# Optimization experiments

Hardware: AMD Instinct MI355X
Metric: run time of the kernel (lower is better)

The kernel has to match this reference:

```python
import jax, jax.numpy as jnp
import numpy as np

FEAT_STRIDE = 16
A = 4  # num anchors (forced by scores.view(-1, K, 4))
FRAMES_PER_VIDEO = 300


def conv2d(x, w, b, pad):
    y = jax.lax.conv_general_dilated(
        x, w, window_strides=(1, 1), padding=[(pad, pad), (pad, pad)],
        dimension_numbers=("NCHW", "OIHW", "NCHW"))
    return y + b[None, :, None, None]


def setup_inputs() -> dict:
    key = jax.random.key(0)
    ks = jax.random.split(key, 8)
    B, C, H, W = 300, 256, 38, 38
    base_feat = jax.random.normal(ks[0], (B, C, H, W), dtype=jnp.float32)
    central_pos = jax.random.randint(ks[1], (1,), 0, FRAMES_PER_VIDEO)
    im_info = jnp.ones((1,), dtype=jnp.float32)
    gt_boxes = jax.random.uniform(ks[2], (1, 4), dtype=jnp.float32)
    # learned params
    W1 = jax.random.normal(ks[3], (128, C, 2, 2), dtype=jnp.float32) * 0.05
    b1 = jnp.zeros((128,), dtype=jnp.float32)
    Wc = jax.random.normal(ks[4], (2 * A, 128, 2, 2), dtype=jnp.float32) * 0.05
    bc = jnp.zeros((2 * A,), dtype=jnp.float32)
    Wb = jax.random.normal(ks[5], (4 * A, 128, 2, 2), dtype=jnp.float32) * 0.05
    bb = jnp.zeros((4 * A,), dtype=jnp.float32)
    anchors = jnp.array([[-8., -8., 8., 8.], [-16., -16., 16., 16.],
                         [-32., -32., 32., 32.], [-64., -64., 64., 64.]],
                        dtype=jnp.float32)
    return {"base_feat": base_feat, "central_pos": central_pos,
            "im_info": im_info, "gt_boxes": gt_boxes,
            "W1": W1, "b1": b1, "Wc": Wc, "bc": bc, "Wb": Wb, "bb": bb,
            "anchors": anchors}


def reference(base_feat, central_pos, im_info, gt_boxes, W1, b1, Wc, bc, Wb, bb, anchors):
    x = jax.nn.relu(conv2d(base_feat, W1, b1, pad=1))          # [B,128,H+1,W+1]
    cls = conv2d(x, Wc, bc, pad=0)                             # [B,2A,H,W]
    B, _, H, Wd = cls.shape
    # torch reshape(x, 2) -> softmax -> reshape back (raw row-major reshapes)
    prob = jax.nn.softmax(cls.reshape(B, 2, A * H, Wd), axis=1).reshape(B, 2 * A, H, Wd)
    scores = prob[:, A:]                                       # [B,A,H,W]
    deltas = conv2d(x, Wb, bb, pad=0)                          # [B,4A,H,W]
    K = H * Wd
    sx = jnp.arange(Wd, dtype=jnp.float32) * FEAT_STRIDE
    sy = jnp.arange(H, dtype=jnp.float32) * FEAT_STRIDE
    gx, gy = jnp.meshgrid(sx, sy)                              # [H,W] each ('xy')
    shifts = jnp.stack([gx.ravel(), gy.ravel(), gx.ravel(), gy.ravel()], axis=1)  # [K,4]
    props = (anchors[None, :, :] + shifts[:, None, :]).reshape(K * A, 4)[None]    # [1,K*A,4]
    d = deltas.transpose(0, 2, 3, 1).reshape(B, K * A, 4)
    proposals = (props + d) * im_info                          # [B,K*A,4]
    # raw reshape of [B,A,H,W] into [B,K,4] (matches .view semantics on a copy)
    sk = scores.reshape(B, K, 4)
    sf = sk.max(axis=2)
    of = sk.argmax(axis=2)                                     # [B,K]
    ss = sf.max(axis=1)
    os_ = sf.argmax(axis=1)                                    # [B]
    bi = jnp.arange(B)
    box_id = os_ * 4 + of[bi, os_]
    boxes = proposals[bi, box_id]                              # [B,4]
    anchor_out = jnp.trunc(boxes / im_info)                    # .int() cast (trunc)
    output = jnp.concatenate([anchor_out, boxes, ss[:, None]], axis=1)  # [B,9]
    # log loss at central frames (vectorized over videos)
    nv = gt_boxes.shape[0]
    idx = FRAMES_PER_VIDEO * jnp.arange(nv) + central_pos
    valid = idx < B
    idxc = jnp.clip(idx, 0, B - 1)
    vb = boxes[idxc]
    vs = ss[idxc]
    # faithful IoU (including the original's max-instead-of-min on xi2/yi2)
    xi1 = jnp.maximum(gt_boxes[:, 0], vb[:, 0])
    yi1 = jnp.maximum(gt_boxes[:, 1], vb[:, 1])
    xi2 = jnp.maximum(gt_boxes[:, 2], vb[:, 2])
    yi2 = jnp.maximum(gt_boxes[:, 3], vb[:, 3])
    inter = (xi2 - xi1) * (yi2 - yi1)
    a1 = (gt_boxes[:, 2] - gt_boxes[:, 0]) * (gt_boxes[:, 3] - gt_boxes[:, 1])
    a2 = (vb[:, 2] - vb[:, 0]) * (vb[:, 3] - vb[:, 1])
    iou = inter / (a1 + a2 - inter)
    lv = jnp.where(iou > 0.7, -jnp.log(vs + 1e-5), -jnp.log(1.0 - vs + 1e-5))
    proposal_loss = jnp.sum(jnp.where(valid, lv, 0.0))
    return output, proposal_loss
```

## Files before the change

kernel.cpp:

```cpp
#include <hip/hip_runtime.h>
#include <math.h>

#define CIN 256
#define HIN 38
#define WIN 38
#define NFRAMES 300
#define COUT1 128
#define P1 1521
#define PSTR 1524
#define HW2 1444
#define NSC 5776
#define CHUNK 75
#define NCHUNKS 4
#define W1F_LO 131072
#define W2F_LO 16384

typedef _Float16 half8 __attribute__((ext_vector_type(8)));
typedef _Float16 half2v __attribute__((ext_vector_type(2)));
typedef float    f32x4 __attribute__((ext_vector_type(4)));

union H2U { unsigned int u; half2v h; };

#define LDS_BAR() do { \
    asm volatile("s_waitcnt lgkmcnt(0)" ::: "memory"); \
    __builtin_amdgcn_s_barrier(); \
    asm volatile("" ::: "memory"); \
} while (0)

__global__ void repack_w1f(const float* __restrict__ W1, _Float16* __restrict__ W1f) {
    int e = blockIdx.x * 256 + threadIdx.x;
    int j  = e & 7;
    int ln = (e >> 3) & 63;
    int mt = (e >> 9) & 7;
    int s  = e >> 12;
    int k  = s * 32 + (ln >> 4) * 8 + j;
    int co = mt * 16 + (ln & 15);
    int kid = k & 3, ci = k >> 2;
    float v = W1[((co * 256) + ci) * 4 + kid] * 64.0f;
    _Float16 h = (_Float16)v;
    W1f[e]          = h;
    W1f[e + W1F_LO] = (_Float16)(v - (float)h);
}

__global__ void repack_w2f(const float* __restrict__ Wc, const float* __restrict__ Wb,
                           _Float16* __restrict__ W2f) {
    int e = blockIdx.x * 256 + threadIdx.x;
    int j  = e & 7;
    int ln = (e >> 3) & 63;
    int mt = (e >> 9) & 1;
    int s  = e >> 10;
    int k  = s * 32 + (ln >> 4) * 8 + j;
    int ch = mt * 16 + (ln & 15);
    int ci = k >> 2, kid = k & 3;
    float v = 0.0f;
    if (ch < 8)       v = Wc[(ch * 128 + ci) * 4 + kid];
    else if (ch < 24) v = Wb[((ch - 8) * 128 + ci) * 4 + kid];
    v *= 64.0f;
    _Float16 h = (_Float16)v;
    W2f[e]          = h;
    W2f[e + W2F_LO] = (_Float16)(v - (float)h);
}

__global__ __launch_bounds__(256, 2) void conv1_mfma(
    const float* __restrict__ bf, const _Float16* __restrict__ W1f,
    const float* __restrict__ b1, unsigned int* __restrict__ xout, int frame0)
{
    __shared__ __align__(16) _Float16 As[16384];
    __shared__ __align__(16) _Float16 Bs[16384];

    const int tid  = threadIdx.x;
    const int wave = tid >> 6, ln = tid & 63;
    const int wrow = wave >> 1, wcol = wave & 1;
    const int fz = blockIdx.y;
    const int b  = frame0 + fz;
    const int p0 = blockIdx.x * 128;
    const float* bfb = bf + (size_t)b * (CIN * HIN * WIN);

    int  addr1[2][8];
    bool kok[2][4];
    int  saddr[2];
#pragma unroll
    for (int r = 0; r < 2; ++r) {
        int slot = tid + r * 256;
        int ln_s = slot & 63, nt = slot >> 6;
        int p = p0 + nt * 16 + (ln_s & 15);
        int quad = ln_s >> 4;
        bool pok = p < P1;
        int pp = pok ? p : 0;
        int h = pp / 39, w = pp - h * 39;
#pragma unroll
        for (int kid = 0; kid < 4; ++kid) {
            int hh = h + (kid >> 1) - 1;
            int ww = w + (kid & 1) - 1;
            kok[r][kid] = pok && ((unsigned)hh < 38u) && ((unsigned)ww < 38u);
            int ko = hh * 38 + ww;
#pragma unroll
            for (int t = 0; t < 2; ++t)
                addr1[r][t * 4 + kid] = quad * 2 * 1444 + t * 1444 + ko;
        }
        saddr[r] = slot * 8;
    }

    f32x4 acc[4][4];
#pragma unroll
    for (int i = 0; i < 4; ++i)
#pragma unroll
        for (int j = 0; j < 4; ++j) acc[i][j] = (f32x4)0.0f;

    float bn0[2][8], bn1[2][8];
    half8 an0[4], an1[4];

#define C1_LOAD(SET, S) do { \
        const float* bsrc_ = bfb + (size_t)(S) * 8 * 1444; \
        _Pragma("unroll") \
        for (int r_ = 0; r_ < 2; ++r_) { \
            _Pragma("unroll") \
            for (int j_ = 0; j_ < 8; ++j_) \
                bn##SET[r_][j_] = kok[r_][j_ & 3] ? bsrc_[addr1[r_][j_]] : 0.0f; \
        } \
        const _Float16* wsl_ = W1f + (size_t)(S) * 4096; \
        _Pragma("unroll") \
        for (int f_ = 0; f_ < 4; ++f_) { \
            int o_ = (tid + f_ * 256) * 8; \
            const _Float16* g_ = (f_ < 2) ? (wsl_ + o_) : (wsl_ + W1F_LO + (o_ - 4096)); \
            an##SET[f_] = *(const half8*)g_; \
        } \
    } while (0)

#define C1_STORE(SET, BUF) do { \
        const int bo_ = (BUF) * 8192; \
        _Pragma("unroll") \
        for (int r_ = 0; r_ < 2; ++r_) { \
            half8 hv_, lv_; \
            _Pragma("unroll") \
            for (int j_ = 0; j_ < 8; ++j_) { \
                float v_ = bn##SET[r_][j_] * 32.0f; \
                _Float16 h_ = (_Float16)v_; \
                hv_[j_] = h_; lv_[j_] = (_Float16)(v_ - (float)h_); \
            } \
            *(half8*)&Bs[bo_ + saddr[r_]] = hv_; \
            *(half8*)&Bs[bo_ + 4096 + saddr[r_]] = lv_; \
        } \
        _Pragma("unroll") \
        for (int f_ = 0; f_ < 4; ++f_) \
            *(half8*)&As[bo_ + (tid + f_ * 256) * 8] = an##SET[f_]; \
    } while (0)

#define C1_COMPUTE(BUF) do { \
        const int bo_ = (BUF) * 8192; \
        half8 af_h[4], af_l[4], bf_h[4], bf_l[4]; \
        _Pragma("unroll") \
        for (int t_ = 0; t_ < 4; ++t_) { \
            int mtile_ = wrow * 4 + t_; \
            af_h[t_] = *(const half8*)&As[bo_ + mtile_ * 512 + ln * 8]; \
            af_l[t_] = *(const half8*)&As[bo_ + 4096 + mtile_ * 512 + ln * 8]; \
            int ntile_ = wcol * 4 + t_; \
            bf_h[t_] = *(const half8*)&Bs[bo_ + (ntile_ * 64 + ln) * 8]; \
            bf_l[t_] = *(const half8*)&Bs[bo_ + 4096 + (ntile_ * 64 + ln) * 8]; \
        } \
        __builtin_amdgcn_s_setprio(1); \
        _Pragma("unroll") \
        for (int i_ = 0; i_ < 4; ++i_) { \
            _Pragma("unroll") \
            for (int j_ = 0; j_ < 4; ++j_) \
                acc[i_][j_] = __builtin_amdgcn_mfma_f32_16x16x32_f16(af_h[i_], bf_h[j_], acc[i_][j_], 0, 0, 0); \
        } \
        _Pragma("unroll") \
        for (int i_ = 0; i_ < 4; ++i_) { \
            _Pragma("unroll") \
            for (int j_ = 0; j_ < 4; ++j_) \
                acc[i_][j_] = __builtin_amdgcn_mfma_f32_16x16x32_f16(af_l[i_], bf_h[j_], acc[i_][j_], 0, 0, 0); \
        } \
        _Pragma("unroll") \
        for (int i_ = 0; i_ < 4; ++i_) { \
            _Pragma("unroll") \
            for (int j_ = 0; j_ < 4; ++j_) \
                acc[i_][j_] = __builtin_amdgcn_mfma_f32_16x16x32_f16(af_h[i_], bf_l[j_], acc[i_][j_], 0, 0, 0); \
        } \
        __builtin_amdgcn_s_setprio(0); \
    } while (0)

    C1_LOAD(0, 0);
    C1_LOAD(1, 1);
    C1_STORE(0, 0);
    LDS_BAR();

    for (int s = 0; s < 32; s += 2) {
        if (s + 2 < 32) C1_LOAD(0, s + 2);
        C1_COMPUTE(0);
        C1_STORE(1, 1);
        LDS_BAR();
        if (s + 3 < 32) C1_LOAD(1, s + 3);
        C1_COMPUTE(1);
        if (s + 2 < 32) {
            C1_STORE(0, 0);
            LDS_BAR();
        }
    }
#undef C1_LOAD
#undef C1_STORE
#undef C1_COMPUTE

    const float sc = 1.0f / 2048.0f;
    const int rq = ln >> 4, cl = ln & 15;
#pragma unroll
    for (int i = 0; i < 4; ++i) {
#pragma unroll
        for (int j = 0; j < 4; ++j) {
            int p = p0 + (wcol * 4 + j) * 16 + cl;
            if (p < P1) {
#pragma unroll
                for (int rr = 0; rr < 4; ++rr) {
                    int co = (wrow * 4 + i) * 16 + rq * 4 + rr;
                    float t = fmaxf(fmaf(acc[i][j][rr], sc, b1[co]), 0.0f) * 32.0f;
                    H2U u;
                    u.h[0] = (_Float16)t;
                    u.h[1] = (_Float16)(t - (float)u.h[0]);
                    xout[((size_t)fz * COUT1 + co) * PSTR + p] = u.u;
                }
            }
        }
    }
}

__global__ __launch_bounds__(256, 2) void stage2_mfma(
    const unsigned int* __restrict__ xq, const _Float16* __restrict__ W2f,
    const float* __restrict__ bcv, const float* __restrict__ bbv,
    float* __restrict__ scores, float* __restrict__ deltas, int frame0)
{
    __shared__ __align__(16) _Float16 Bs[16384];
    __shared__ float clsb[8][128];

    const int tid  = threadIdx.x;
    const int wave = tid >> 6, ln = tid & 63;
    const int fz = blockIdx.y;
    const int b  = frame0 + fz;
    const int p0 = blockIdx.x * 128;
    const unsigned int* xb = xq + (size_t)fz * COUT1 * PSTR;

    int  addr2[2][8];
    bool sok[2];
    int  saddr[2];
#pragma unroll
    for (int r = 0; r < 2; ++r) {
        int slot = tid + r * 256;
        int ln_s = slot & 63, nt = slot >> 6;
        int p = p0 + nt * 16 + (ln_s & 15);
        int quad = ln_s >> 4;
        sok[r] = p < HW2;
        int pp = sok[r] ? p : 0;
        int h = pp / 38, w = pp - h * 38;
#pragma unroll
        for (int kid = 0; kid < 4; ++kid) {
            int ko = (h + (kid >> 1)) * 39 + (w + (kid & 1));
#pragma unroll
            for (int t = 0; t < 2; ++t)
                addr2[r][t * 4 + kid] = (quad * 2 + t) * PSTR + ko;
        }
        saddr[r] = slot * 8;
    }

    f32x4 acc[2][2];
    acc[0][0] = (f32x4)0.0f; acc[0][1] = (f32x4)0.0f;
    acc[1][0] = (f32x4)0.0f; acc[1][1] = (f32x4)0.0f;

    unsigned int bu0[2][8], bu1[2][8];
    half8 a0_h[2], a0_l[2], a1_h[2], a1_l[2];

#define S2_LOADB(SET, S) do { \
        const unsigned int* row_ = xb + (size_t)(S) * 8 * PSTR; \
        _Pragma("unroll") \
        for (int r_ = 0; r_ < 2; ++r_) { \
            _Pragma("unroll") \
            for (int j_ = 0; j_ < 8; ++j_) \
                bu##SET[r_][j_] = sok[r_] ? row_[addr2[r_][j_]] : 0u; \
        } \
    } while (0)

#define S2_LOADA(SET, S) do { \
        _Pragma("unroll") \
        for (int mt_ = 0; mt_ < 2; ++mt_) { \
            const _Float16* wp_ = W2f + ((size_t)((S) * 2 + mt_) * 64 + ln) * 8; \
            a##SET##_h[mt_] = *(const half8*)wp_; \
            a##SET##_l[mt_] = *(const half8*)(wp_ + W2F_LO); \
        } \
    } while (0)

#define S2_STORE(SET, BUF) do { \
        const int bo_ = (BUF) * 8192; \
        _Pragma("unroll") \
        for (int r_ = 0; r_ < 2; ++r_) { \
            half8 hv_, lv_; \
            _Pragma("unroll") \
            for (int j_ = 0; j_ < 8; ++j_) { \
                H2U t_; t_.u = bu##SET[r_][j_]; \
                hv_[j_] = t_.h[0]; lv_[j_] = t_.h[1]; \
            } \
            *(half8*)&Bs[bo_ + saddr[r_]] = hv_; \
            *(half8*)&Bs[bo_ + 4096 + saddr[r_]] = lv_; \
        } \
    } while (0)

#define S2_COMPUTE(SET, BUF) do { \
        const int bo_ = (BUF) * 8192; \
        half8 b_h[2], b_l[2]; \
        _Pragma("unroll") \
        for (int t_ = 0; t_ < 2; ++t_) { \
            int ntile_ = wave * 2 + t_; \
            b_h[t_] = *(const half8*)&Bs[bo_ + (ntile_ * 64 + ln) * 8]; \
            b_l[t_] = *(const half8*)&Bs[bo_ + 4096 + (ntile_ * 64 + ln) * 8]; \
        } \
        __builtin_amdgcn_s_setprio(1); \
        _Pragma("unroll") \
        for (int i_ = 0; i_ < 2; ++i_) { \
            _Pragma("unroll") \
            for (int j_ = 0; j_ < 2; ++j_) \
                acc[i_][j_] = __builtin_amdgcn_mfma_f32_16x16x32_f16(a##SET##_h[i_], b_h[j_], acc[i_][j_], 0, 0, 0); \
        } \
        _Pragma("unroll") \
        for (int i_ = 0; i_ < 2; ++i_) { \
            _Pragma("unroll") \
            for (int j_ = 0; j_ < 2; ++j_) \
                acc[i_][j_] = __builtin_amdgcn_mfma_f32_16x16x32_f16(a##SET##_l[i_], b_h[j_], acc[i_][j_], 0, 0, 0); \
        } \
        _Pragma("unroll") \
        for (int i_ = 0; i_ < 2; ++i_) { \
            _Pragma("unroll") \
            for (int j_ = 0; j_ < 2; ++j_) \
                acc[i_][j_] = __builtin_amdgcn_mfma_f32_16x16x32_f16(a##SET##_h[i_], b_l[j_], acc[i_][j_], 0, 0, 0); \
        } \
        __builtin_amdgcn_s_setprio(0); \
    } while (0)

    S2_LOADB(0, 0);
    S2_LOADA(0, 0);
    S2_LOADB(1, 1);
    S2_LOADA(1, 1);
    S2_STORE(0, 0);
    LDS_BAR();

    for (int s = 0; s < 16; s += 2) {
        if (s + 2 < 16) S2_LOADB(0, s + 2);
        S2_COMPUTE(0, 0);
        S2_STORE(1, 1);
        if (s + 2 < 16) S2_LOADA(0, s + 2);
        LDS_BAR();
        if (s + 3 < 16) S2_LOADB(1, s + 3);
        S2_COMPUTE(1, 1);
        if (s + 2 < 16) {
            S2_STORE(0, 0);
            if (s + 3 < 16) S2_LOADA(1, s + 3);
            LDS_BAR();
        }
    }
#undef S2_LOADB
#undef S2_LOADA
#undef S2_STORE
#undef S2_COMPUTE

    const float sc = 1.0f / 2048.0f;
    const int rq = ln >> 4, cl = ln & 15;
#pragma unroll
    for (int mt = 0; mt < 2; ++mt) {
#pragma unroll
        for (int t = 0; t < 2; ++t) {
            int lpx = (wave * 2 + t) * 16 + cl;
            int p = p0 + lpx;
#pragma unroll
            for (int rr = 0; rr < 4; ++rr) {
                int ch = mt * 16 + rq * 4 + rr;
                float v = acc[mt][t][rr] * sc;
                if (ch < 8) {
                    clsb[ch][lpx] = v + bcv[ch];
                } else if (ch < 24 && p < HW2) {
                    deltas[((size_t)b * 16 + (ch - 8)) * HW2 + p] = v + bbv[ch - 8];
                }
            }
        }
    }
    __syncthreads();

    for (int e = tid; e < 512; e += 256) {
        int a = e >> 7, lp = e & 127;
        int p = p0 + lp;
        if (p < HW2) {
            float z1 = clsb[a][lp];
            float z2 = clsb[a + 4][lp];
            float mx = fmaxf(z1, z2);
            float e1 = expf(z1 - mx), e2 = expf(z2 - mx);
            scores[(size_t)b * NSC + a * HW2 + p] = e2 / (e1 + e2);
        }
    }
}

__global__ __launch_bounds__(256) void argmax_kernel(
    const float* __restrict__ scores, const float* __restrict__ deltas,
    const float* __restrict__ anchors, const float* __restrict__ im_info,
    float* __restrict__ out, float* __restrict__ boxesb, float* __restrict__ ssb)
{
    const int b = blockIdx.x, tid = threadIdx.x;
    const float* s = scores + (size_t)b * NSC;
    float best = -INFINITY;
    int bidx = 0;
    for (int i = tid; i < NSC; i += 256) {
        float v = s[i];
        if (v > best) { best = v; bidx = i; }
    }
    __shared__ float sv[256];
    __shared__ int   si[256];
    sv[tid] = best; si[tid] = bidx;
    __syncthreads();
    for (int stp = 128; stp > 0; stp >>= 1) {
        if (tid < stp) {
            float ov = sv[tid + stp]; int oi = si[tid + stp];
            if (ov > sv[tid] || (ov == sv[tid] && oi < si[tid])) { sv[tid] = ov; si[tid] = oi; }
        }
        __syncthreads();
    }
    if (tid == 0) {
        float ss = sv[0];
        int id = si[0];
        int kprime = id >> 2, aprime = id & 3;
        int hp = kprime / 38, wp = kprime - hp * 38;
        float im = im_info[0];
        float gx = (float)wp * 16.0f, gy = (float)hp * 16.0f;
#pragma unroll
        for (int j = 0; j < 4; ++j) {
            float shift = ((j & 1) == 0) ? gx : gy;
            float prop = anchors[aprime * 4 + j] + shift;
            float dlt = deltas[((size_t)b * 16 + (aprime * 4 + j)) * HW2 + kprime];
            float bx = (prop + dlt) * im;
            out[b * 9 + j]     = truncf(bx / im);
            out[b * 9 + 4 + j] = bx;
            boxesb[b * 4 + j]  = bx;
        }
        out[b * 9 + 8] = ss;
        ssb[b] = ss;
    }
}

__global__ void loss_kernel(const int* __restrict__ central_pos,
                            const float* __restrict__ gt,
                            const float* __restrict__ boxesb,
                            const float* __restrict__ ssb,
                            float* __restrict__ out)
{
    if (threadIdx.x != 0 || blockIdx.x != 0) return;
    int idx = central_pos[0];
    bool valid = idx < NFRAMES;
    int idxc = min(max(idx, 0), NFRAMES - 1);
    float vb0 = boxesb[idxc * 4 + 0], vb1 = boxesb[idxc * 4 + 1];
    float vb2 = boxesb[idxc * 4 + 2], vb3 = boxesb[idxc * 4 + 3];
    float vs = ssb[idxc];
    float g0 = gt[0], g1 = gt[1], g2 = gt[2], g3 = gt[3];
    float xi1 = fmaxf(g0, vb0), yi1 = fmaxf(g1, vb1);
    float xi2 = fmaxf(g2, vb2), yi2 = fmaxf(g3, vb3);
    float inter = (xi2 - xi1) * (yi2 - yi1);
    float a1 = (g2 - g0) * (g3 - g1);
    float a2 = (vb2 - vb0) * (vb3 - vb1);
    float iou = inter / (a1 + a2 - inter);
    float lv = (iou > 0.7f) ? -logf(vs + 1e-5f) : -logf(1.0f - vs + 1e-5f);
    out[NFRAMES * 9] = valid ? lv : 0.0f;
}

extern "C" void kernel_launch(void* const* d_in, const int* in_sizes, int n_in,
                              void* d_out, int out_size, void* d_ws, size_t ws_size,
                              hipStream_t stream) {
    const float* base_feat   = (const float*)d_in[0];
    const int*   central_pos = (const int*)d_in[1];
    const float* im_info     = (const float*)d_in[2];
    const float* gt_boxes    = (const float*)d_in[3];
    const float* W1 = (const float*)d_in[4];
    const float* b1 = (const float*)d_in[5];
    const float* Wc = (const float*)d_in[6];
    const float* bc = (const float*)d_in[7];
    const float* Wb = (const float*)d_in[8];
    const float* bb = (const float*)d_in[9];
    const float* anchors = (const float*)d_in[10];
    float* out = (float*)d_out;

    float* p = (float*)d_ws;
    unsigned int* xbuf = (unsigned int*)p; p += (size_t)CHUNK * COUT1 * PSTR;
    float* scores = p;  p += (size_t)NFRAMES * NSC;
    float* deltas = p;  p += (size_t)NFRAMES * 16 * HW2;
    _Float16* w1f = (_Float16*)p; p += 131072;
    _Float16* w2f = (_Float16*)p; p += 16384;
    float* boxesb = p;  p += NFRAMES * 4;
    float* ssb    = p;

    repack_w1f<<<512, 256, 0, stream>>>(W1, w1f);
    repack_w2f<<<64, 256, 0, stream>>>(Wc, Wb, w2f);

    for (int c = 0; c < NCHUNKS; ++c) {
        int f0 = c * CHUNK;
        conv1_mfma<<<dim3(12, CHUNK), 256, 0, stream>>>(base_feat, w1f, b1, xbuf, f0);
        stage2_mfma<<<dim3(12, CHUNK), 256, 0, stream>>>(xbuf, w2f, bc, bb, scores, deltas, f0);
    }
    argmax_kernel<<<NFRAMES, 256, 0, stream>>>(scores, deltas, anchors, im_info, out, boxesb, ssb);
    loss_kernel<<<1, 64, 0, stream>>>(central_pos, gt_boxes, boxesb, ssb, out);
}
```

Before: 1.119 ms.

## Load conv1 weight fragments directly from global into registers, skip LDS staging

The conv1 MFMA kernel no longer stages the pre-swizzled weight tiles through shared memory. Each wave loads its A fragments (high and low fp16 halves) straight from global memory into registers, and the compute loop reads B per n-tile. This halves conv1's LDS footprint, so launch bounds go up to 3 blocks per CU for conv1 and 4 for stage2. The trade-offs are more global weight traffic per wave, loads that are now less far ahead of their use, and tighter register limits that could cause spills.

```diff
diff --git a/kernel.cpp b/kernel.cpp
--- a/kernel.cpp
+++ b/kernel.cpp
@@ -61,11 +61,10 @@
     W2f[e + W2F_LO] = (_Float16)(v - (float)h);
 }
 
-__global__ __launch_bounds__(256, 2) void conv1_mfma(
+__global__ __launch_bounds__(256, 3) void conv1_mfma(
     const float* __restrict__ bf, const _Float16* __restrict__ W1f,
     const float* __restrict__ b1, unsigned int* __restrict__ xout, int frame0)
 {
-    __shared__ __align__(16) _Float16 As[16384];
     __shared__ __align__(16) _Float16 Bs[16384];
 
     const int tid  = threadIdx.x;
@@ -75,6 +74,7 @@
     const int b  = frame0 + fz;
     const int p0 = blockIdx.x * 128;
     const float* bfb = bf + (size_t)b * (CIN * HIN * WIN);
+    const _Float16* wbase = W1f + (size_t)wrow * 2048 + (size_t)ln * 8;
 
     int  addr1[2][8];
     bool kok[2][4];
@@ -108,9 +108,18 @@
         for (int j = 0; j < 4; ++j) acc[i][j] = (f32x4)0.0f;
 
     float bn0[2][8], bn1[2][8];
-    half8 an0[4], an1[4];
-
-#define C1_LOAD(SET, S) do { \
+    half8 ah[4], al[4];
+
+#define C1_LOADA(S) do { \
+        const _Float16* wsl_ = wbase + (size_t)(S) * 4096; \
+        _Pragma("unroll") \
+        for (int t_ = 0; t_ < 4; ++t_) { \
+            ah[t_] = *(const half8*)(wsl_ + t_ * 512); \
+            al[t_] = *(const half8*)(wsl_ + W1F_LO + t_ * 512); \
+        } \
+    } while (0)
+
+#define C1_LOADB(SET, S) do { \
         const float* bsrc_ = bfb + (size_t)(S) * 8 * 1444; \
         _Pragma("unroll") \
         for (int r_ = 0; r_ < 2; ++r_) { \
@@ -118,16 +127,9 @@
             for (int j_ = 0; j_ < 8; ++j_) \
                 bn##SET[r_][j_] = kok[r_][j_ & 3] ? bsrc_[addr1[r_][j_]] : 0.0f; \
         } \
-        const _Float16* wsl_ = W1f + (size_t)(S) * 4096; \
-        _Pragma("unroll") \
-        for (int f_ = 0; f_ < 4; ++f_) { \
-            int o_ = (tid + f_ * 256) * 8; \
-            const _Float16* g_ = (f_ < 2) ? (wsl_ + o_) : (wsl_ + W1F_LO + (o_ - 4096)); \
-            an##SET[f_] = *(const half8*)g_; \
-        } \
-    } while (0)
-
-#define C1_STORE(SET, BUF) do { \
+    } while (0)
+
+#define C1_STOREB(SET, BUF) do { \
         const int bo_ = (BUF) * 8192; \
         _Pragma("unroll") \
         for (int r_ = 0; r_ < 2; ++r_) { \
@@ -141,64 +143,52 @@
             *(half8*)&Bs[bo_ + saddr[r_]] = hv_; \
             *(half8*)&Bs[bo_ + 4096 + saddr[r_]] = lv_; \
         } \
-        _Pragma("unroll") \
-        for (int f_ = 0; f_ < 4; ++f_) \
-            *(half8*)&As[bo_ + (tid + f_ * 256) * 8] = an##SET[f_]; \
     } while (0)
 
 #define C1_COMPUTE(BUF) do { \
         const int bo_ = (BUF) * 8192; \
-        half8 af_h[4], af_l[4], bf_h[4], bf_l[4]; \
-        _Pragma("unroll") \
-        for (int t_ = 0; t_ < 4; ++t_) { \
-            int mtile_ = wrow * 4 + t_; \
-            af_h[t_] = *(const half8*)&As[bo_ + mtile_ * 512 + ln * 8]; \
-            af_l[t_] = *(const half8*)&As[bo_ + 4096 + mtile_ * 512 + ln * 8]; \
-            int ntile_ = wcol * 4 + t_; \
-            bf_h[t_] = *(const half8*)&Bs[bo_ + (ntile_ * 64 + ln) * 8]; \
-            bf_l[t_] = *(const half8*)&Bs[bo_ + 4096 + (ntile_ * 64 + ln) * 8]; \
-        } \
-        __builtin_amdgcn_s_setprio(1); \
-        _Pragma("unroll") \
-        for (int i_ = 0; i_ < 4; ++i_) { \
-            _Pragma("unroll") \
-            for (int j_ = 0; j_ < 4; ++j_) \
-                acc[i_][j_] = __builtin_amdgcn_mfma_f32_16x16x32_f16(af_h[i_], bf_h[j_], acc[i_][j_], 0, 0, 0); \
-        } \
-        _Pragma("unroll") \
-        for (int i_ = 0; i_ < 4; ++i_) { \
-            _Pragma("unroll") \
-            for (int j_ = 0; j_ < 4; ++j_) \
-                acc[i_][j_] = __builtin_amdgcn_mfma_f32_16x16x32_f16(af_l[i_], bf_h[j_], acc[i_][j_], 0, 0, 0); \
-        } \
-        _Pragma("unroll") \
-        for (int i_ = 0; i_ < 4; ++i_) { \
-            _Pragma("unroll") \
-            for (int j_ = 0; j_ < 4; ++j_) \
-                acc[i_][j_] = __builtin_amdgcn_mfma_f32_16x16x32_f16(af_h[i_], bf_l[j_], acc[i_][j_], 0, 0, 0); \
-        } \
-        __builtin_amdgcn_s_setprio(0); \
-    } while (0)
-
-    C1_LOAD(0, 0);
-    C1_LOAD(1, 1);
-    C1_STORE(0, 0);
+        _Pragma("unroll") \
+        for (int j_ = 0; j_ < 4; ++j_) { \
+            int ntile_ = wcol * 4 + j_; \
+            half8 bh_ = *(const half8*)&Bs[bo_ + (ntile_ * 64 + ln) * 8]; \
+            half8 bl_ = *(const half8*)&Bs[bo_ + 4096 + (ntile_ * 64 + ln) * 8]; \
+            __builtin_amdgcn_s_setprio(1); \
+            _Pragma("unroll") \
+            for (int i_ = 0; i_ < 4; ++i_) \
+                acc[i_][j_] = __builtin_amdgcn_mfma_f32_16x16x32_f16(ah[i_], bh_, acc[i_][j_], 0, 0, 0); \
+            _Pragma("unroll") \
+            for (int i_ = 0; i_ < 4; ++i_) \
+                acc[i_][j_] = __builtin_amdgcn_mfma_f32_16x16x32_f16(al[i_], bh_, acc[i_][j_], 0, 0, 0); \
+            _Pragma("unroll") \
+            for (int i_ = 0; i_ < 4; ++i_) \
+                acc[i_][j_] = __builtin_amdgcn_mfma_f32_16x16x32_f16(ah[i_], bl_, acc[i_][j_], 0, 0, 0); \
+            __builtin_amdgcn_s_setprio(0); \
+        } \
+    } while (0)
+
+    C1_LOADA(0);
+    C1_LOADB(0, 0);
+    C1_LOADB(1, 1);
+    C1_STOREB(0, 0);
     LDS_BAR();
 
     for (int s = 0; s < 32; s += 2) {
-        if (s + 2 < 32) C1_LOAD(0, s + 2);
         C1_COMPUTE(0);
-        C1_STORE(1, 1);
+        C1_LOADA(s + 1);
+        if (s + 2 < 32) C1_LOADB(0, s + 2);
+        C1_STOREB(1, 1);
         LDS_BAR();
-        if (s + 3 < 32) C1_LOAD(1, s + 3);
         C1_COMPUTE(1);
         if (s + 2 < 32) {
-            C1_STORE(0, 0);
+            C1_LOADA(s + 2);
+            if (s + 3 < 32) C1_LOADB(1, s + 3);
+            C1_STOREB(0, 0);
             LDS_BAR();
         }
     }
-#undef C1_LOAD
-#undef C1_STORE
+#undef C1_LOADA
+#undef C1_LOADB
+#undef C1_STOREB
 #undef C1_COMPUTE
 
     const float sc = 1.0f / 2048.0f;
@@ -223,7 +213,7 @@
     }
 }
 
-__global__ __launch_bounds__(256, 2) void stage2_mfma(
+__global__ __launch_bounds__(256, 4) void stage2_mfma(
     const unsigned int* __restrict__ xq, const _Float16* __restrict__ W2f,
     const float* __restrict__ bcv, const float* __restrict__ bbv,
     float* __restrict__ scores, float* __restrict__ deltas, int frame0)
```

Measured after the change: 1.604 ms. 1.43x slower.

## Stage input row tile in LDS and gather im2col from shared memory

Applied to the files above, without the earlier changes.

Conv1 used to gather im2col values straight from global memory with 16 scattered, redundant loads per thread per k-step. It now loads a contiguous tile of the input (8 channels by 6 rows by 38 columns) into a double-buffered LDS array with coalesced loads, then does the im2col gather from LDS when building the fp16 hi/lo B tiles. This is meant to cut redundant, uncoalesced global traffic. In exchange it adds 16 KB of LDS per block, which may reduce occupancy, and extra LDS reads and barrier dependencies.

```diff
diff --git a/kernel.cpp b/kernel.cpp
--- a/kernel.cpp
+++ b/kernel.cpp
@@ -67,6 +67,7 @@
 {
     __shared__ __align__(16) _Float16 As[16384];
     __shared__ __align__(16) _Float16 Bs[16384];
+    __shared__ __align__(16) float    Xs[4096];
 
     const int tid  = threadIdx.x;
     const int wave = tid >> 6, ln = tid & 63;
@@ -75,8 +76,10 @@
     const int b  = frame0 + fz;
     const int p0 = blockIdx.x * 128;
     const float* bfb = bf + (size_t)b * (CIN * HIN * WIN);
-
-    int  addr1[2][8];
+    const int h_top   = p0 / 39;
+    const int r_first = h_top - 1;
+
+    int  tix[2][8];
     bool kok[2][4];
     int  saddr[2];
 #pragma unroll
@@ -92,32 +95,41 @@
         for (int kid = 0; kid < 4; ++kid) {
             int hh = h + (kid >> 1) - 1;
             int ww = w + (kid & 1) - 1;
-            kok[r][kid] = pok && ((unsigned)hh < 38u) && ((unsigned)ww < 38u);
-            int ko = hh * 38 + ww;
-#pragma unroll
-            for (int t = 0; t < 2; ++t)
-                addr1[r][t * 4 + kid] = quad * 2 * 1444 + t * 1444 + ko;
+            bool ok = pok && ((unsigned)hh < 38u) && ((unsigned)ww < 38u);
+            kok[r][kid] = ok;
+            int rr = (h - h_top) + (kid >> 1);
+#pragma unroll
+            for (int t = 0; t < 2; ++t) {
+                int ix = (quad * 2 + t) * 228 + rr * 38 + ww;
+                tix[r][t * 4 + kid] = ok ? ix : 0;
+            }
         }
         saddr[r] = slot * 8;
     }
 
+    int tgo[8];
+#pragma unroll
+    for (int it = 0; it < 8; ++it) {
+        int e = tid + it * 256;
+        int ch = e / 228;
+        int rem = e - ch * 228;
+        int rr = rem / 38;
+        int col = rem - rr * 38;
+        int hh = r_first + rr;
+        bool ok = (e < 1824) && ((unsigned)hh < 38u);
+        tgo[it] = ok ? (ch * 1444 + hh * 38 + col) : -1;
+    }
+
     f32x4 acc[4][4];
 #pragma unroll
     for (int i = 0; i < 4; ++i)
 #pragma unroll
         for (int j = 0; j < 4; ++j) acc[i][j] = (f32x4)0.0f;
 
-    float bn0[2][8], bn1[2][8];
     half8 an0[4], an1[4];
-
-#define C1_LOAD(SET, S) do { \
-        const float* bsrc_ = bfb + (size_t)(S) * 8 * 1444; \
-        _Pragma("unroll") \
-        for (int r_ = 0; r_ < 2; ++r_) { \
-            _Pragma("unroll") \
-            for (int j_ = 0; j_ < 8; ++j_) \
-                bn##SET[r_][j_] = kok[r_][j_ & 3] ? bsrc_[addr1[r_][j_]] : 0.0f; \
-        } \
+    float treg[8];
+
+#define C1_ALOAD(SET, S) do { \
         const _Float16* wsl_ = W1f + (size_t)(S) * 4096; \
         _Pragma("unroll") \
         for (int f_ = 0; f_ < 4; ++f_) { \
@@ -127,23 +139,40 @@
         } \
     } while (0)
 
-#define C1_STORE(SET, BUF) do { \
+#define C1_ASTORE(SET, BUF) do { \
+        _Pragma("unroll") \
+        for (int f_ = 0; f_ < 4; ++f_) \
+            *(half8*)&As[(BUF) * 8192 + (tid + f_ * 256) * 8] = an##SET[f_]; \
+    } while (0)
+
+#define C1_TLOAD(S) do { \
+        const float* bsrc_ = bfb + (size_t)(S) * 8 * 1444; \
+        _Pragma("unroll") \
+        for (int it_ = 0; it_ < 8; ++it_) \
+            treg[it_] = (tgo[it_] >= 0) ? bsrc_[tgo[it_]] : 0.0f; \
+    } while (0)
+
+#define C1_TSTORE(XB) do { \
+        _Pragma("unroll") \
+        for (int it_ = 0; it_ < 8; ++it_) \
+            Xs[(XB) * 2048 + tid + it_ * 256] = treg[it_]; \
+    } while (0)
+
+#define C1_GATHER(BUF, XB) do { \
         const int bo_ = (BUF) * 8192; \
         _Pragma("unroll") \
         for (int r_ = 0; r_ < 2; ++r_) { \
             half8 hv_, lv_; \
             _Pragma("unroll") \
             for (int j_ = 0; j_ < 8; ++j_) { \
-                float v_ = bn##SET[r_][j_] * 32.0f; \
+                float v0_ = kok[r_][j_ & 3] ? Xs[(XB) * 2048 + tix[r_][j_]] : 0.0f; \
+                float v_ = v0_ * 32.0f; \
                 _Float16 h_ = (_Float16)v_; \
                 hv_[j_] = h_; lv_[j_] = (_Float16)(v_ - (float)h_); \
             } \
             *(half8*)&Bs[bo_ + saddr[r_]] = hv_; \
             *(half8*)&Bs[bo_ + 4096 + saddr[r_]] = lv_; \
         } \
-        _Pragma("unroll") \
-        for (int f_ = 0; f_ < 4; ++f_) \
-            *(half8*)&As[bo_ + (tid + f_ * 256) * 8] = an##SET[f_]; \
     } while (0)
 
 #define C1_COMPUTE(BUF) do { \
@@ -180,25 +209,38 @@
         __builtin_amdgcn_s_setprio(0); \
     } while (0)
 
-    C1_LOAD(0, 0);
-    C1_LOAD(1, 1);
-    C1_STORE(0, 0);
+    C1_ALOAD(0, 0);
+    C1_TLOAD(0);
+    C1_TSTORE(0);
+    C1_ALOAD(1, 1);
+    C1_TLOAD(1);
+    C1_TSTORE(1);
     LDS_BAR();
+    C1_GATHER(0, 0);
+    C1_ASTORE(0, 0);
+    LDS_BAR();
 
     for (int s = 0; s < 32; s += 2) {
-        if (s + 2 < 32) C1_LOAD(0, s + 2);
+        if (s + 2 < 32) { C1_ALOAD(0, s + 2); C1_TLOAD(s + 2); }
         C1_COMPUTE(0);
-        C1_STORE(1, 1);
+        C1_GATHER(1, 1);
+        C1_ASTORE(1, 1);
+        if (s + 2 < 32) C1_TSTORE(0);
         LDS_BAR();
-        if (s + 3 < 32) C1_LOAD(1, s + 3);
+        if (s + 3 < 32) { C1_ALOAD(1, s + 3); C1_TLOAD(s + 3); }
         C1_COMPUTE(1);
         if (s + 2 < 32) {
-            C1_STORE(0, 0);
+            C1_GATHER(0, 0);
+            C1_ASTORE(0, 0);
+            if (s + 3 < 32) C1_TSTORE(1);
             LDS_BAR();
         }
     }
-#undef C1_LOAD
-#undef C1_STORE
+#undef C1_ALOAD
+#undef C1_ASTORE
+#undef C1_TLOAD
+#undef C1_TSTORE
+#undef C1_GATHER
 #undef C1_COMPUTE
 
     const float sc = 1.0f / 2048.0f;
```

After: 1.207 ms. 1.08x slower.
